# Kernel tuning notes

Hardware: AMD Instinct MI355X
Metric: run time of the kernel (lower is better)

The kernel has to match this reference:

```python
import jax, jax.numpy as jnp
import numpy as np

N_NODES = 100000
N_EDGES = 1600000
D_IN = 100      # entity/relation embedding dim (rel_weight is [100,50])
D_HID = 50      # conv1 out_channels (hard-coded in ctor)
N_REL = 237     # relation_num; rel_embedding doubled -> 474 relation types
N_REL2 = 2 * N_REL
N_BASES = 5     # num_bases hard-coded
N_CLASS = 50    # class_num


def setup_inputs() -> dict:
    key = jax.random.key(0)
    ks = jax.random.split(key, 12)
    x = jax.random.normal(ks[0], (N_NODES, D_IN), dtype=jnp.float32)
    edge_index = jax.random.randint(ks[1], (2, N_EDGES), 0, N_NODES)
    edge_type = jax.random.randint(ks[2], (N_EDGES,), 0, N_REL2)
    rel_embedding = jax.random.normal(ks[3], (N_REL, D_IN), dtype=jnp.float32) * 0.1
    rel_weight = jax.random.uniform(ks[4], (D_IN, D_HID), dtype=jnp.float32)  # nn.Parameter(torch.rand)
    basis1 = jax.random.normal(ks[5], (N_BASES, D_IN, D_HID), dtype=jnp.float32) * 0.1
    comp1 = jax.random.normal(ks[6], (N_REL2, N_BASES), dtype=jnp.float32) * 0.1
    root1 = jax.random.normal(ks[7], (D_IN, D_HID), dtype=jnp.float32) * 0.1
    bias1 = jnp.zeros((D_HID,), dtype=jnp.float32)
    basis2 = jax.random.normal(ks[8], (N_BASES, D_HID, N_CLASS), dtype=jnp.float32) * 0.1
    comp2 = jax.random.normal(ks[9], (N_REL2, N_BASES), dtype=jnp.float32) * 0.1
    root2 = jax.random.normal(ks[10], (D_HID, N_CLASS), dtype=jnp.float32) * 0.1
    bias2 = jnp.zeros((N_CLASS,), dtype=jnp.float32)
    return {
        "x": x, "edge_index": edge_index, "edge_type": edge_type, "target_node": 5,
        "rel_embedding": rel_embedding, "rel_weight": rel_weight,
        "basis1": basis1, "comp1": comp1, "root1": root1, "bias1": bias1,
        "basis2": basis2, "comp2": comp2, "root2": root2, "bias2": bias2,
    }


def _transe_conv(x, src, dst, e_emb, comp_e, basis, root_w, bias):
    """RGCN-style conv with TransE compose and basis decomposition.
    x: [N, Fin], e_emb: [E, Fin], comp_e: [E, B], basis: [B, Fin, Fout].
    message m = x[src] + e_emb; out_e = m @ (sum_b comp_e[b] * basis[b]); mean-agg at dst.
    """
    m = x[src] + e_emb  # [E, Fin] -- dominant gather
    acc = jnp.zeros((m.shape[0], basis.shape[2]), dtype=m.dtype)
    for b in range(basis.shape[0]):  # small fixed basis count (5)
        acc = acc + comp_e[:, b:b + 1] * (m @ basis[b])
    agg = jax.ops.segment_sum(acc, dst, num_segments=x.shape[0])  # [N, Fout]
    cnt = jax.ops.segment_sum(jnp.ones((dst.shape[0],), dtype=x.dtype), dst,
                              num_segments=x.shape[0])
    mean = agg / jnp.maximum(cnt, 1.0)[:, None]
    return mean + x @ root_w + bias


def reference(x, edge_index, edge_type, target_node, rel_embedding, rel_weight,
              basis1, comp1, root1, bias1, basis2, comp2, root2, bias2):
    # x[target_node] = 0
    x = x.at[target_node].set(0.0)
    src, dst = edge_index[0], edge_index[1]
    # rel_embedding doubled (forward + inverse relations)
    rel_full = jnp.concatenate([rel_embedding, rel_embedding], axis=0)  # [2R, D_IN]
    e1 = rel_full[edge_type]                                            # [E, D_IN]
    h = _transe_conv(x, src, dst, e1, comp1[edge_type], basis1, root1, bias1)
    rel2 = rel_full @ rel_weight                                        # [2R, D_HID]
    e2 = rel2[edge_type]                                                # [E, D_HID]
    h = _transe_conv(h, src, dst, e2, comp2[edge_type], basis2, root2, bias2)
    return jax.nn.log_softmax(h, axis=1)
```

## Files before the change

kernel.cpp:

```cpp
#include <hip/hip_runtime.h>
#include <hip/hip_bf16.h>

typedef __hip_bfloat16 bf16;

#define N_NODES 100000
#define N_EDGES 1600000
#define D_IN    100
#define D_HID   50
#define N_REL   237
#define N_REL2  474
#define N_CLASS 50

#define NBUCK    196
#define BSHIFT   9
#define BCAP     10240
#define BIN_EPB  1024
#define BIN_BLKS ((N_EDGES + BIN_EPB - 1) / BIN_EPB)

#define MID_PACK1_BLKS 160
#define MID_PACK2_BLKS 80
#define MID_REL_BLKS   474
#define MID_TOTAL (BIN_BLKS + MID_PACK1_BLKS + MID_PACK2_BLKS + MID_REL_BLKS)

#define GEMM_BLKS ((N_NODES + 31) / 32)

#define CST 324

#define RED_BLKS (N_NODES / 8)

typedef __attribute__((ext_vector_type(8))) short short8;
typedef __attribute__((ext_vector_type(4))) float f32x4;
typedef __attribute__((ext_vector_type(2))) float f32x2;

__device__ __forceinline__ float b2f(bf16 v) { return __bfloat162float(v); }
__device__ __forceinline__ bf16  f2b(float v) { return __float2bfloat16(v); }

__device__ __forceinline__ float ldw(const void* p, int idx, int isbf) {
    return isbf ? b2f(((const bf16*)p)[idx]) : ((const float*)p)[idx];
}

#if __has_builtin(__builtin_amdgcn_cvt_f32_fp8) && __has_builtin(__builtin_amdgcn_cvt_pk_fp8_f32)
#define F8_HW 1
#endif
#if __has_builtin(__builtin_amdgcn_cvt_pk_f32_fp8)
#define F8PK_HW 1
#endif

__device__ __forceinline__ float f8tof(unsigned u) {
#ifdef F8_HW
    return __builtin_amdgcn_cvt_f32_fp8((int)u, 0);
#else
    unsigned s = u >> 7, e = (u >> 3) & 0xF, m = u & 7;
    float v;
    if (e == 0) v = (float)m * 0.001953125f;
    else        v = (float)(8 + m) * __builtin_ldexpf(1.f, (int)e - 10);
    return s ? -v : v;
#endif
}

#ifdef F8_HW
#define F8SEL(u, s) __builtin_amdgcn_cvt_f32_fp8((int)(u), (s))
#else
#define F8SEL(u, s) f8tof(((u) >> (8 * (s))) & 0xFFu)
#endif

template <bool HI>
__device__ __forceinline__ f32x2 f8pk(unsigned u) {
#ifdef F8PK_HW
    return __builtin_amdgcn_cvt_pk_f32_fp8((int)u, HI);
#else
    f32x2 r;
    r.x = F8SEL(u, HI ? 2 : 0);
    r.y = F8SEL(u, HI ? 3 : 1);
    return r;
#endif
}

__device__ __forceinline__ unsigned f8enc_sw(float v) {
    unsigned bits = __float_as_uint(v);
    unsigned s = bits >> 31;
    float a = fabsf(v);
    if (a < 0.0009765625f) return s << 7;
    if (a >= 448.f) return (s << 7) | 0x7E;
    int E = (int)((bits >> 23) & 0xFF) - 127;
    unsigned m = bits & 0x7FFFFF;
    if (E < -6) {
        int q = (int)rintf(a * 512.f);
        if (q > 7) q = 7;
        return (s << 7) | (unsigned)q;
    }
    unsigned lsb = (m >> 20) & 1, rnd = (m >> 19) & 1;
    unsigned sticky = (m & 0x7FFFF) ? 1u : 0u;
    unsigned m3 = (m >> 20) + (rnd & (sticky | lsb));
    if (m3 == 8) { m3 = 0; E += 1; }
    if (E > 8) return (s << 7) | 0x7E;
    return (s << 7) | ((unsigned)(E + 7) << 3) | m3;
}

__device__ __forceinline__ unsigned pk4_f8(float v0, float v1, float v2, float v3) {
#ifdef F8_HW
    int p = __builtin_amdgcn_cvt_pk_fp8_f32(v0, v1, 0, false);
    p = __builtin_amdgcn_cvt_pk_fp8_f32(v2, v3, p, true);
    return (unsigned)p;
#else
    return f8enc_sw(v0) | (f8enc_sw(v1) << 8) | (f8enc_sw(v2) << 16) | (f8enc_sw(v3) << 24);
#endif
}

__global__ void k_detect(const unsigned short* __restrict__ xr, int* __restrict__ flag) {
    int tid = threadIdx.x;
    int cnt = 0;
    for (int i = tid; i < 4096; i += 256) {
        unsigned short u = xr[2 * i];
        unsigned e = (u >> 7) & 0xFF;
        bool pl = (e >= 107 && e <= 132) || ((u & 0x7FFF) == 0);
        cnt += pl ? 1 : 0;
    }
    __shared__ int sh[256];
    sh[tid] = cnt;
    __syncthreads();
    for (int s = 128; s > 0; s >>= 1) {
        if (tid < s) sh[tid] += sh[tid + s];
        __syncthreads();
    }
    if (tid == 0) flag[0] = (sh[0] >= 3072) ? 1 : 0;
}

__device__ __forceinline__ void job_bin(int blk, const int* __restrict__ src,
                                        const int* __restrict__ dst,
                                        const int* __restrict__ et,
                                        unsigned* __restrict__ bucketFill,
                                        unsigned long long* __restrict__ staging) {
    __shared__ unsigned lhist[NBUCK];
    __shared__ unsigned lstart[NBUCK];
    __shared__ unsigned gbase[NBUCK];
    __shared__ unsigned scan_tmp[NBUCK];
    __shared__ unsigned long long lval[BIN_EPB];
    __shared__ unsigned ltgt[BIN_EPB];
    int tid = threadIdx.x;
    int base = blk * BIN_EPB;
    int n = N_EDGES - base; if (n > BIN_EPB) n = BIN_EPB;

    for (int i = tid; i < NBUCK; i += 256) lhist[i] = 0;
    __syncthreads();

    unsigned bb[4], rr[4];
    unsigned long long vv[4];
#pragma unroll
    for (int j = 0; j < 4; ++j) {
        int i = j * 256 + tid;
        bb[j] = 0xFFFFFFFFu;
        if (i < n) {
            int e = base + i;
            unsigned d = (unsigned)dst[e];
            unsigned b = d >> BSHIFT;
            bb[j] = b;
            rr[j] = atomicAdd(&lhist[b], 1u);
            vv[j] = ((unsigned long long)d << 32) |
                    (unsigned long long)((unsigned)src[e] | ((unsigned)et[e] << 17));
        }
    }
    __syncthreads();
    unsigned v0 = (tid < NBUCK) ? lhist[tid] : 0;
    if (tid < NBUCK) scan_tmp[tid] = v0;
    __syncthreads();
    for (int s = 1; s < NBUCK; s <<= 1) {
        unsigned t = 0;
        if (tid < NBUCK && tid >= (unsigned)s) t = scan_tmp[tid - s];
        __syncthreads();
        if (tid < NBUCK) scan_tmp[tid] += t;
        __syncthreads();
    }
    if (tid < NBUCK) {
        lstart[tid] = scan_tmp[tid] - v0;
        gbase[tid] = (v0 > 0) ? atomicAdd(&bucketFill[tid], v0) : 0u;
    }
    __syncthreads();
#pragma unroll
    for (int j = 0; j < 4; ++j) {
        if (bb[j] != 0xFFFFFFFFu) {
            unsigned pos = lstart[bb[j]] + rr[j];
            unsigned off = gbase[bb[j]] + rr[j];
            lval[pos] = vv[j];
            ltgt[pos] = (off < BCAP) ? (bb[j] * BCAP + off) : 0xFFFFFFFFu;
        }
    }
    __syncthreads();
    for (int i = tid; i < n; i += 256) {
        unsigned t = ltgt[i];
        if (t != 0xFFFFFFFFu) staging[t] = lval[i];
    }
}

__device__ __forceinline__ void job_pack(int blk, const void* basis, const void* root,
                                         bf16* Wb, int KL, int isbf) {
    int g = blk * 256 + threadIdx.x;
    int ks = g / 10240;
    int r = g - ks * 10240;
    int ct = r >> 9;
    int r2 = r & 511;
    int l = r2 >> 3, j = r2 & 7;
    int k = ks * 32 + ((l >> 4) << 3) + j;
    int n = ct * 16 + (l & 15);
    float v = 0.f;
    if (k < KL && n < 300) {
        if (n < 250) { int b = n / 50, f = n - b * 50; v = ldw(basis, (b * KL + k) * 50 + f, isbf); }
        else         v = ldw(root, k * 50 + (n - 250), isbf);
    }
    Wb[g] = f2b(v);
}

template<int ISBF>
__device__ __forceinline__ void job_rel(int t,
        const void* __restrict__ rel_emb, const void* __restrict__ rel_w,
        const void* __restrict__ basis1, const void* __restrict__ comp1,
        const void* __restrict__ basis2, const void* __restrict__ comp2,
        float* __restrict__ rt1, float* __restrict__ rt2,
        float* __restrict__ c81, float* __restrict__ c82) {
    int tid = threadIdx.x;
    __shared__ float rf[D_IN];
    __shared__ float r2s[D_HID];
    int tm = (t >= N_REL) ? t - N_REL : t;
    if (tid < D_IN) rf[tid] = ldw(rel_emb, tm * D_IN + tid, ISBF);
    if (tid < 8) {
        c81[t * 8 + tid] = (tid < 5) ? ldw(comp1, t * 5 + tid, ISBF) : 0.f;
        c82[t * 8 + tid] = (tid < 5) ? ldw(comp2, t * 5 + tid, ISBF) : 0.f;
    }
    __syncthreads();
    if (tid < 50) {
        int f = tid;
        float a = 0.f;
        for (int b = 0; b < 5; ++b) {
            float cb = ldw(comp1, t * 5 + b, ISBF);
            float s = 0.f;
            for (int k = 0; k < D_IN; ++k) s += rf[k] * ldw(basis1, (b * D_IN + k) * 50 + f, ISBF);
            a += cb * s;
        }
        rt1[t * 50 + f] = a;
        float s2 = 0.f;
        for (int k = 0; k < D_IN; ++k) s2 += rf[k] * ldw(rel_w, k * 50 + f, ISBF);
        r2s[f] = s2;
    }
    __syncthreads();
    if (tid < 50) {
        int f = tid;
        float a = 0.f;
        for (int b = 0; b < 5; ++b) {
            float cb = ldw(comp2, t * 5 + b, ISBF);
            float s = 0.f;
            for (int k = 0; k < 50; ++k) s += r2s[k] * ldw(basis2, (b * 50 + k) * 50 + f, ISBF);
            a += cb * s;
        }
        rt2[t * 50 + f] = a;
    }
}

__global__ __launch_bounds__(256) void k_mid(const int* __restrict__ srcp,
                                             const int* __restrict__ dstp,
                                             const int* __restrict__ etp,
                                             unsigned* __restrict__ bucketFill,
                                             unsigned long long* __restrict__ staging,
                                             const int* __restrict__ flag,
                                             const void* rel_emb, const void* rel_w,
                                             const void* basis1, const void* comp1,
                                             const void* root1,
                                             const void* basis2, const void* comp2,
                                             const void* root2,
                                             bf16* __restrict__ Wb1, bf16* __restrict__ Wb2,
                                             float* __restrict__ rt1, float* __restrict__ rt2,
                                             float* __restrict__ c81, float* __restrict__ c82) {
    int blk = blockIdx.x;
    if (blk < BIN_BLKS) { job_bin(blk, srcp, dstp, etp, bucketFill, staging); return; }
    blk -= BIN_BLKS;
    int isbf = flag[0];
    if (blk < MID_PACK1_BLKS) { job_pack(blk, basis1, root1, Wb1, D_IN, isbf); return; }
    blk -= MID_PACK1_BLKS;
    if (blk < MID_PACK2_BLKS) { job_pack(blk, basis2, root2, Wb2, D_HID, isbf); return; }
    blk -= MID_PACK2_BLKS;
    if (isbf) job_rel<1>(blk, rel_emb, rel_w, basis1, comp1, basis2, comp2, rt1, rt2, c81, c82);
    else      job_rel<0>(blk, rel_emb, rel_w, basis1, comp1, basis2, comp2, rt1, rt2, c81, c82);
}

__device__ __forceinline__ void job_bucket(int b, char* shraw,
        const unsigned long long* __restrict__ staging,
        const unsigned* __restrict__ bucketFill,
        int* __restrict__ offs, unsigned* __restrict__ se) {
    unsigned* hist = (unsigned*)shraw;
    unsigned* excl = hist + 512;
    unsigned* bfs  = excl + 512;
    unsigned* tmp  = bfs + 256;
    int tid = threadIdx.x;

    if (tid < NBUCK) {
        unsigned c = bucketFill[tid];
        bfs[tid] = (c > BCAP) ? BCAP : c;
    }
    hist[tid] = 0; hist[tid + 256] = 0;
    __syncthreads();
    for (int s = 1; s < NBUCK; s <<= 1) {
        unsigned t = 0;
        if (tid < NBUCK && tid >= s) t = bfs[tid - s];
        __syncthreads();
        if (tid < NBUCK) bfs[tid] += t;
        __syncthreads();
    }
    unsigned base = (b == 0) ? 0u : bfs[b - 1];
    unsigned cnt = bfs[b] - base;

    const unsigned long long* p = staging + (size_t)b * BCAP;
    for (unsigned i = tid; i < cnt; i += 256) {
        unsigned d = (unsigned)(p[i] >> 32);
        atomicAdd(&hist[d & 511], 1u);
    }
    __syncthreads();
    unsigned h0 = hist[2 * tid], h1 = hist[2 * tid + 1];
    tmp[tid] = h0 + h1;
    __syncthreads();
    for (int s = 1; s < 256; s <<= 1) {
        unsigned t = (tid >= s) ? tmp[tid - s] : 0u;
        __syncthreads();
        tmp[tid] += t;
        __syncthreads();
    }
    unsigned pe = (tid > 0) ? tmp[tid - 1] : 0u;
    excl[2 * tid]     = pe;
    excl[2 * tid + 1] = pe + h0;
    hist[2 * tid] = 0; hist[2 * tid + 1] = 0;
    __syncthreads();

#pragma unroll
    for (int q = 0; q < 2; ++q) {
        int li = 2 * tid + q;
        int node = b * 512 + li;
        if (node < N_NODES) offs[node] = (int)(base + excl[li]);
        if (node == N_NODES - 1) offs[N_NODES] = (int)(base + cnt);
    }

    for (unsigned i = tid; i < cnt; i += 256) {
        unsigned long long v = p[i];
        unsigned ld = ((unsigned)(v >> 32)) & 511u;
        unsigned r = atomicAdd(&hist[ld], 1u);
        se[base + excl[ld] + r] = (unsigned)v;
    }
}

template<int KP, bool ZT, bool RAWX>
__global__ __launch_bounds__(256, 4) void k_gemm_b(const void* __restrict__ Xraw,
                                                const int* __restrict__ flag,
                                                const bf16* __restrict__ Wb,
                                                unsigned char* __restrict__ Y8,
                                                bf16* __restrict__ R, int M,
                                                const int* __restrict__ tgt,
                                                const unsigned long long* __restrict__ staging,
                                                const unsigned* __restrict__ bucketFill,
                                                int* __restrict__ offs,
                                                unsigned* __restrict__ se,
                                                int nbuckBlks) {
    constexpr int AP = KP + 8;
    constexpr int CBYTES = 32 * CST * 2;
    constexpr int ABYTES = 32 * AP * 2;
    __shared__ __attribute__((aligned(16))) char shraw[CBYTES + ABYTES];
    if ((int)blockIdx.x < nbuckBlks) {
        job_bucket(blockIdx.x, shraw, staging, bucketFill, offs, se);
        return;
    }
    int gblk = blockIdx.x - nbuckBlks;
    bf16* smemC = (bf16*)shraw;
    bf16* smemA = (bf16*)(shraw + CBYTES);
    int tid = threadIdx.x;
    int w = tid >> 6, lane = tid & 63;
    int quad = lane >> 4, cIn = lane & 15;
    int rw = w & 1, cw = w >> 1;
    int base_row = gblk * 32;

    if (RAWX) {
        int isbf = flag[0];
        for (int i = tid; i < 32 * 64; i += 256) {
            int r = i >> 6, c2 = (i & 63) << 1;
            int row = base_row + r; if (row > M - 1) row = M - 1;
            unsigned pkd = 0;
            if (c2 < 100) {
                if (isbf) {
                    pkd = *(const unsigned*)((const unsigned short*)Xraw + (size_t)row * 100 + c2);
                } else {
                    const float* xp = (const float*)Xraw + (size_t)row * 100 + c2;
                    float vx = xp[0], vy = xp[1];
                    bf16 b0 = f2b(vx), b1 = f2b(vy);
                    pkd = (unsigned)*(unsigned short*)&b0 | ((unsigned)*(unsigned short*)&b1 << 16);
                }
            }
            *(unsigned*)(&smemA[r * AP + c2]) = pkd;
        }
    } else {
        const bf16* X = (const bf16*)Xraw;
        const int TOT = 32 * KP / 8;
        for (int i = tid; i < TOT; i += 256) {
            int e8 = i * 8;
            int r = e8 / KP, c = e8 - r * KP;
            int row = base_row + r; if (row > M - 1) row = M - 1;
            *(uint4*)(&smemA[r * AP + c]) = *(const uint4*)(&X[(size_t)row * KP + c]);
        }
    }
    __syncthreads();

    f32x4 acc[10];
#pragma unroll
    for (int i = 0; i < 10; ++i) acc[i] = (f32x4){0.f, 0.f, 0.f, 0.f};

#pragma unroll
    for (int ks = 0; ks < KP / 32; ++ks) {
        short8 a = *(const short8*)(&smemA[(rw * 16 + cIn) * AP + ks * 32 + quad * 8]);
#pragma unroll
        for (int ct = 0; ct < 10; ++ct) {
            short8 b = *(const short8*)(&Wb[(size_t)((ks * 20 + cw * 10 + ct) * 64 + lane) * 8]);
            acc[ct] = __builtin_amdgcn_mfma_f32_16x16x32_bf16(a, b, acc[ct], 0, 0, 0);
        }
    }

#pragma unroll
    for (int ct = 0; ct < 10; ++ct)
#pragma unroll
        for (int r = 0; r < 4; ++r)
            smemC[(rw * 16 + quad * 4 + r) * CST + (cw * 10 + ct) * 16 + cIn] = f2b(acc[ct][r]);
    __syncthreads();

    int tv = -1;
    if (ZT) tv = tgt[0];
    int valid = M - base_row; if (valid > 32) valid = 32;

    for (int i = tid; i < valid * 64; i += 256) {
        int r = i >> 6, u = i & 63;
        int row = base_row + r;
        unsigned pbits;
        if (u < 50) {
            pbits = pk4_f8(b2f(smemC[r * CST + u]),       b2f(smemC[r * CST + 50 + u]),
                           b2f(smemC[r * CST + 100 + u]), b2f(smemC[r * CST + 150 + u]));
        } else if (u < 63) {
            int fb = (u - 50) * 4;
            float v0 = (fb + 0 < 50) ? b2f(smemC[r * CST + 200 + fb + 0]) : 0.f;
            float v1 = (fb + 1 < 50) ? b2f(smemC[r * CST + 200 + fb + 1]) : 0.f;
            float v2 = (fb + 2 < 50) ? b2f(smemC[r * CST + 200 + fb + 2]) : 0.f;
            float v3 = (fb + 3 < 50) ? b2f(smemC[r * CST + 200 + fb + 3]) : 0.f;
            pbits = pk4_f8(v0, v1, v2, v3);
        } else {
            pbits = 0u;
        }
        if (ZT && row == tv) pbits = 0u;
        *(unsigned*)(Y8 + (size_t)row * 256 + u * 4) = pbits;
    }
    for (int i = tid; i < valid * 32; i += 256) {
        int r = i >> 5, cu = i & 31;
        int row = base_row + r;
        int j0 = cu * 2, j1 = j0 + 1;
        unsigned short ua = (j0 < 50) ? *(const unsigned short*)&smemC[r * CST + 250 + j0] : 0;
        unsigned short ub = (j1 < 50) ? *(const unsigned short*)&smemC[r * CST + 250 + j1] : 0;
        unsigned u = (unsigned)ua | ((unsigned)ub << 16);
        if (ZT && row == tv) u = 0u;
        *(unsigned*)((unsigned short*)R + (size_t)row * 64 + j0) = u;
    }
}

__device__ __forceinline__ void edge_body(unsigned p, int f,
        const unsigned char* __restrict__ Y8,
        const float* __restrict__ c8, const float* __restrict__ rt,
        f32x2& acc2, float& accS) {
    unsigned ps = (unsigned)__builtin_amdgcn_readfirstlane((int)p);
    int s_ = (int)(ps & 0x1FFFFu);
    int t_ = (int)(ps >> 17);
    const unsigned char* yr = Y8 + (size_t)s_ * 256;
    unsigned a4 = *(const unsigned*)(yr + 4 * f);
    float y4 = f8tof(yr[200 + f]);
    const float* cp = c8 + t_ * 8;
    f32x4 c03 = *(const f32x4*)cp;
    float c4 = cp[4];
    float rv = rt[t_ * 50 + f];
    f32x2 y01 = f8pk<false>(a4);
    f32x2 y23 = f8pk<true>(a4);
    f32x2 cA; cA.x = c03.x; cA.y = c03.y;
    f32x2 cB; cB.x = c03.z; cB.y = c03.w;
    acc2 += cA * y01;
    acc2 += cB * y23;
    accS += rv + c4 * y4;
}

__device__ __forceinline__ void pair_reduce(const int* __restrict__ off,
        const unsigned int* __restrict__ se, const float* __restrict__ c8,
        const float* __restrict__ rt, const unsigned char* __restrict__ Y8,
        int rowA, int f, float& outA, float& outB, float& cntA, float& cntB) {
    int e0 = __builtin_amdgcn_readfirstlane(off[rowA]);
    int e1 = __builtin_amdgcn_readfirstlane(off[rowA + 1]);
    int e2 = __builtin_amdgcn_readfirstlane(off[rowA + 2]);
    f32x2 a2A; a2A.x = 0.f; a2A.y = 0.f;
    f32x2 a2B; a2B.x = 0.f; a2B.y = 0.f;
    float sA = 0.f, sB = 0.f;
    int eA = e0, eB = e1;
    while (eA + 4 <= e1 && eB + 4 <= e2) {
        unsigned pA0 = se[eA],     pA1 = se[eA + 1], pA2 = se[eA + 2], pA3 = se[eA + 3];
        unsigned pB0 = se[eB],     pB1 = se[eB + 1], pB2 = se[eB + 2], pB3 = se[eB + 3];
        edge_body(pA0, f, Y8, c8, rt, a2A, sA);
        edge_body(pB0, f, Y8, c8, rt, a2B, sB);
        edge_body(pA1, f, Y8, c8, rt, a2A, sA);
        edge_body(pB1, f, Y8, c8, rt, a2B, sB);
        edge_body(pA2, f, Y8, c8, rt, a2A, sA);
        edge_body(pB2, f, Y8, c8, rt, a2B, sB);
        edge_body(pA3, f, Y8, c8, rt, a2A, sA);
        edge_body(pB3, f, Y8, c8, rt, a2B, sB);
        eA += 4; eB += 4;
    }
    while (eA + 4 <= e1) {
        unsigned p0 = se[eA], p1 = se[eA + 1], p2 = se[eA + 2], p3 = se[eA + 3];
        edge_body(p0, f, Y8, c8, rt, a2A, sA);
        edge_body(p1, f, Y8, c8, rt, a2A, sA);
        edge_body(p2, f, Y8, c8, rt, a2A, sA);
        edge_body(p3, f, Y8, c8, rt, a2A, sA);
        eA += 4;
    }
    while (eB + 4 <= e2) {
        unsigned p0 = se[eB], p1 = se[eB + 1], p2 = se[eB + 2], p3 = se[eB + 3];
        edge_body(p0, f, Y8, c8, rt, a2B, sB);
        edge_body(p1, f, Y8, c8, rt, a2B, sB);
        edge_body(p2, f, Y8, c8, rt, a2B, sB);
        edge_body(p3, f, Y8, c8, rt, a2B, sB);
        eB += 4;
    }
    for (; eA < e1; ++eA) edge_body(se[eA], f, Y8, c8, rt, a2A, sA);
    for (; eB < e2; ++eB) edge_body(se[eB], f, Y8, c8, rt, a2B, sB);
    outA = a2A.x + a2A.y + sA;
    outB = a2B.x + a2B.y + sB;
    float nA = (float)(e1 - e0); cntA = nA > 1.f ? nA : 1.f;
    float nB = (float)(e2 - e1); cntB = nB > 1.f ? nB : 1.f;
}

__global__ __launch_bounds__(256) void k_reduce1(const int* __restrict__ off,
                                                 const unsigned int* __restrict__ se,
                                                 const float* __restrict__ c8,
                                                 const float* __restrict__ rt,
                                                 const unsigned char* __restrict__ Y8,
                                                 const bf16* __restrict__ R,
                                                 const void* __restrict__ bias_raw,
                                                 const int* __restrict__ flag,
                                                 bf16* __restrict__ h) {
    int wid = threadIdx.x >> 6, lane = threadIdx.x & 63;
    int rowA = __builtin_amdgcn_readfirstlane(blockIdx.x * 8 + wid * 2);
    int f = (lane < 50) ? lane : 49;
    float accA, accB, cntA, cntB;
    pair_reduce(off, se, c8, rt, Y8, rowA, f, accA, accB, cntA, cntB);
    float bv = ldw(bias_raw, f, flag[0]);
    float vA = accA / cntA + b2f(R[(size_t)rowA * 64 + f]) + bv;
    float vB = accB / cntB + b2f(R[(size_t)(rowA + 1) * 64 + f]) + bv;
    h[(size_t)rowA * 64 + lane]       = f2b(lane < 50 ? vA : 0.f);
    h[(size_t)(rowA + 1) * 64 + lane] = f2b(lane < 50 ? vB : 0.f);
}

__device__ __forceinline__ void softmax_store(float acc, float cnt, int row, int f,
        int lane, const bf16* __restrict__ R, float bv,
        int isbf, void* __restrict__ out) {
    float v = -INFINITY;
    if (lane < 50)
        v = acc / cnt + b2f(R[(size_t)row * 64 + f]) + bv;
    float m = v;
    for (int o = 32; o > 0; o >>= 1) m = fmaxf(m, __shfl_xor(m, o));
    float ex = (lane < 50) ? expf(v - m) : 0.f;
    float s = ex;
    for (int o = 32; o > 0; o >>= 1) s += __shfl_xor(s, o);
    float res = v - m - logf(s);
    if (lane < 50) {
        if (isbf) ((bf16*)out)[row * 50 + f] = f2b(res);
        else      ((float*)out)[row * 50 + f] = res;
    }
}

__global__ __launch_bounds__(256) void k_reduce2(const int* __restrict__ off,
                                                 const unsigned int* __restrict__ se,
                                                 const float* __restrict__ c8,
                                                 const float* __restrict__ rt,
                                                 const unsigned char* __restrict__ Y8,
                                                 const bf16* __restrict__ R,
                                                 const void* __restrict__ bias_raw,
                                                 const int* __restrict__ flag,
                                                 void* __restrict__ out) {
    int wid = threadIdx.x >> 6, lane = threadIdx.x & 63;
    int rowA = __builtin_amdgcn_readfirstlane(blockIdx.x * 8 + wid * 2);
    int f = (lane < 50) ? lane : 49;
    float accA, accB, cntA, cntB;
    pair_reduce(off, se, c8, rt, Y8, rowA, f, accA, accB, cntA, cntB);
    int isbf = flag[0];
    float bv = ldw(bias_raw, f, isbf);
    softmax_store(accA, cntA, rowA, f, lane, R, bv, isbf, out);
    softmax_store(accB, cntB, rowA + 1, f, lane, R, bv, isbf, out);
}

extern "C" void kernel_launch(void* const* d_in, const int* in_sizes, int n_in,
                              void* d_out, int out_size, void* d_ws, size_t ws_size,
                              hipStream_t stream) {
    const void* x_raw = d_in[0];
    const int*  ei    = (const int*)d_in[1];
    const int*  et    = (const int*)d_in[2];
    const int*  tgt   = (const int*)d_in[3];
    const void* rel_emb = d_in[4];
    const void* rel_w   = d_in[5];
    const void* basis1  = d_in[6];
    const void* comp1   = d_in[7];
    const void* root1   = d_in[8];
    const void* bias1   = d_in[9];
    const void* basis2  = d_in[10];
    const void* comp2   = d_in[11];
    const void* root2   = d_in[12];
    const void* bias2   = d_in[13];

    char* wsp = (char*)d_ws;
    size_t off_b = 0;
    auto alloc = [&](size_t bytes) {
        void* p = wsp + off_b;
        off_b = (off_b + bytes + 255) & ~(size_t)255;
        return p;
    };
    unsigned char* Y8 = (unsigned char*)alloc((size_t)N_NODES * 256);
    bf16*  R    = (bf16*) alloc((size_t)N_NODES * 64 * sizeof(bf16));
    bf16*  h    = (bf16*) alloc((size_t)N_NODES * 64 * sizeof(bf16));
    unsigned int* se = (unsigned int*)alloc((size_t)N_EDGES * sizeof(unsigned int));
    unsigned long long* staging = (unsigned long long*)alloc((size_t)NBUCK * BCAP * 8);
    int*   offs = (int*)  alloc((size_t)(N_NODES + 1) * sizeof(int));
    unsigned* bucketFill = (unsigned*)alloc((size_t)NBUCK * sizeof(unsigned));
    bf16*  Wb1  = (bf16*) alloc((size_t)40960 * sizeof(bf16));
    bf16*  Wb2  = (bf16*) alloc((size_t)20480 * sizeof(bf16));
    float* rt1  = (float*)alloc((size_t)N_REL2 * 50 * sizeof(float));
    float* rt2  = (float*)alloc((size_t)N_REL2 * 50 * sizeof(float));
    float* c81  = (float*)alloc((size_t)N_REL2 * 8 * sizeof(float));
    float* c82  = (float*)alloc((size_t)N_REL2 * 8 * sizeof(float));
    int*   flag = (int*)  alloc(sizeof(int));

    const int* srcp = ei;
    const int* dstp = ei + N_EDGES;

    hipMemsetAsync(bucketFill, 0, (size_t)NBUCK * sizeof(unsigned), stream);

    k_detect<<<1, 256, 0, stream>>>((const unsigned short*)x_raw, flag);

    k_mid<<<MID_TOTAL, 256, 0, stream>>>(srcp, dstp, et, bucketFill, staging, flag,
                                         rel_emb, rel_w, basis1, comp1, root1,
                                         basis2, comp2, root2,
                                         Wb1, Wb2, rt1, rt2, c81, c82);

    k_gemm_b<128, true, true><<<GEMM_BLKS + NBUCK, 256, 0, stream>>>(
        x_raw, flag, Wb1, Y8, R, N_NODES, tgt, staging, bucketFill, offs, se, NBUCK);

    k_reduce1<<<RED_BLKS, 256, 0, stream>>>(offs, se, c81, rt1, Y8, R, bias1, flag, h);

    k_gemm_b<64, false, false><<<GEMM_BLKS, 256, 0, stream>>>(
        h, flag, Wb2, Y8, R, N_NODES, nullptr, staging, bucketFill, offs, se, 0);

    k_reduce2<<<RED_BLKS, 256, 0, stream>>>(offs, se, c82, rt2, Y8, R, bias2, flag, d_out);
}
```

Before: 360.9 us.

## Fuse layer-1 mean aggregation with layer-2 basis GEMM into one kernel

Adds a 1024-thread kernel that runs the layer-1 edge reduction for 32 rows, keeps the resulting hidden activations in shared memory, and immediately multiplies them by the layer-2 basis weights with MFMA. It writes the fp8 Y and bf16 root outputs into separate ping-pong buffers, so no reads of layer-1 buffers are overwritten. This removes the global write and read of h and one kernel launch. The cost is extra workspace, used only when it fits, and large blocks that may limit occupancy during the latency-bound gather phase.

```diff
diff --git a/kernel.cpp b/kernel.cpp
--- a/kernel.cpp
+++ b/kernel.cpp
@@ -552,6 +552,89 @@
     h[(size_t)(rowA + 1) * 64 + lane] = f2b(lane < 50 ? vB : 0.f);
 }
 
+__global__ __launch_bounds__(1024) void k_fused(const int* __restrict__ off,
+                                                const unsigned int* __restrict__ se,
+                                                const float* __restrict__ c8,
+                                                const float* __restrict__ rt,
+                                                const unsigned char* __restrict__ Y8in,
+                                                const bf16* __restrict__ Rin,
+                                                const void* __restrict__ bias_raw,
+                                                const int* __restrict__ flag,
+                                                const bf16* __restrict__ Wb,
+                                                unsigned char* __restrict__ Y8out,
+                                                bf16* __restrict__ Rout) {
+    constexpr int HP = 72;
+    __shared__ __attribute__((aligned(16))) char shraw[32 * HP * 2 + 32 * CST * 2];
+    bf16* hT    = (bf16*)shraw;
+    bf16* smemC = (bf16*)(shraw + 32 * HP * 2);
+    int tid = threadIdx.x;
+    int wid = tid >> 6, lane = tid & 63;
+    int quad = lane >> 4, cIn = lane & 15;
+    int base_row = blockIdx.x * 32;
+    int rowA = __builtin_amdgcn_readfirstlane(base_row + wid * 2);
+    int f = (lane < 50) ? lane : 49;
+
+    float accA, accB, cntA, cntB;
+    pair_reduce(off, se, c8, rt, Y8in, rowA, f, accA, accB, cntA, cntB);
+    float bv = ldw(bias_raw, f, flag[0]);
+    float vA = accA / cntA + b2f(Rin[(size_t)rowA * 64 + f]) + bv;
+    float vB = accB / cntB + b2f(Rin[(size_t)(rowA + 1) * 64 + f]) + bv;
+    hT[(wid * 2) * HP + lane]     = f2b(lane < 50 ? vA : 0.f);
+    hT[(wid * 2 + 1) * HP + lane] = f2b(lane < 50 ? vB : 0.f);
+    __syncthreads();
+
+    if (wid < 8) {
+        int rw = wid & 1, cs = wid >> 1;
+        f32x4 acc[5];
+#pragma unroll
+        for (int i = 0; i < 5; ++i) acc[i] = (f32x4){0.f, 0.f, 0.f, 0.f};
+#pragma unroll
+        for (int ks = 0; ks < 2; ++ks) {
+            short8 a = *(const short8*)(&hT[(rw * 16 + cIn) * HP + ks * 32 + quad * 8]);
+#pragma unroll
+            for (int j = 0; j < 5; ++j) {
+                short8 b = *(const short8*)(&Wb[(size_t)((ks * 20 + cs * 5 + j) * 64 + lane) * 8]);
+                acc[j] = __builtin_amdgcn_mfma_f32_16x16x32_bf16(a, b, acc[j], 0, 0, 0);
+            }
+        }
+#pragma unroll
+        for (int j = 0; j < 5; ++j)
+#pragma unroll
+            for (int r = 0; r < 4; ++r)
+                smemC[(rw * 16 + quad * 4 + r) * CST + (cs * 5 + j) * 16 + cIn] = f2b(acc[j][r]);
+    }
+    __syncthreads();
+
+    for (int i = tid; i < 32 * 64; i += 1024) {
+        int r = i >> 6, u = i & 63;
+        int row = base_row + r;
+        unsigned pbits;
+        if (u < 50) {
+            pbits = pk4_f8(b2f(smemC[r * CST + u]),       b2f(smemC[r * CST + 50 + u]),
+                           b2f(smemC[r * CST + 100 + u]), b2f(smemC[r * CST + 150 + u]));
+        } else if (u < 63) {
+            int fb = (u - 50) * 4;
+            float v0 = (fb + 0 < 50) ? b2f(smemC[r * CST + 200 + fb + 0]) : 0.f;
+            float v1 = (fb + 1 < 50) ? b2f(smemC[r * CST + 200 + fb + 1]) : 0.f;
+            float v2 = (fb + 2 < 50) ? b2f(smemC[r * CST + 200 + fb + 2]) : 0.f;
+            float v3 = (fb + 3 < 50) ? b2f(smemC[r * CST + 200 + fb + 3]) : 0.f;
+            pbits = pk4_f8(v0, v1, v2, v3);
+        } else {
+            pbits = 0u;
+        }
+        *(unsigned*)(Y8out + (size_t)row * 256 + u * 4) = pbits;
+    }
+    for (int i = tid; i < 32 * 32; i += 1024) {
+        int r = i >> 5, cu = i & 31;
+        int row = base_row + r;
+        int j0 = cu * 2, j1 = j0 + 1;
+        unsigned short ua = (j0 < 50) ? *(const unsigned short*)&smemC[r * CST + 250 + j0] : 0;
+        unsigned short ub = (j1 < 50) ? *(const unsigned short*)&smemC[r * CST + 250 + j1] : 0;
+        unsigned u = (unsigned)ua | ((unsigned)ub << 16);
+        *(unsigned*)((unsigned short*)Rout + (size_t)row * 64 + j0) = u;
+    }
+}
+
 __device__ __forceinline__ void softmax_store(float acc, float cnt, int row, int f,
         int lane, const bf16* __restrict__ R, float bv,
         int isbf, void* __restrict__ out) {
@@ -617,7 +700,6 @@
     };
     unsigned char* Y8 = (unsigned char*)alloc((size_t)N_NODES * 256);
     bf16*  R    = (bf16*) alloc((size_t)N_NODES * 64 * sizeof(bf16));
-    bf16*  h    = (bf16*) alloc((size_t)N_NODES * 64 * sizeof(bf16));
     unsigned int* se = (unsigned int*)alloc((size_t)N_EDGES * sizeof(unsigned int));
     unsigned long long* staging = (unsigned long long*)alloc((size_t)NBUCK * BCAP * 8);
     int*   offs = (int*)  alloc((size_t)(N_NODES + 1) * sizeof(int));
@@ -630,6 +712,16 @@
     float* c82  = (float*)alloc((size_t)N_REL2 * 8 * sizeof(float));
     int*   flag = (int*)  alloc(sizeof(int));
 
+    size_t fusedExtra = (size_t)N_NODES * 256 + 512 + (size_t)N_NODES * 64 * 2 + 512;
+    bool useFused = (off_b + fusedExtra <= ws_size);
+    unsigned char* Y8b = nullptr; bf16* Rb = nullptr; bf16* h = nullptr;
+    if (useFused) {
+        Y8b = (unsigned char*)alloc((size_t)N_NODES * 256);
+        Rb  = (bf16*)alloc((size_t)N_NODES * 64 * sizeof(bf16));
+    } else {
+        h   = (bf16*)alloc((size_t)N_NODES * 64 * sizeof(bf16));
+    }
+
     const int* srcp = ei;
     const int* dstp = ei + N_EDGES;
 
@@ -645,10 +737,14 @@
     k_gemm_b<128, true, true><<<GEMM_BLKS + NBUCK, 256, 0, stream>>>(
         x_raw, flag, Wb1, Y8, R, N_NODES, tgt, staging, bucketFill, offs, se, NBUCK);
 
-    k_reduce1<<<RED_BLKS, 256, 0, stream>>>(offs, se, c81, rt1, Y8, R, bias1, flag, h);
-
-    k_gemm_b<64, false, false><<<GEMM_BLKS, 256, 0, stream>>>(
-        h, flag, Wb2, Y8, R, N_NODES, nullptr, staging, bucketFill, offs, se, 0);
-
-    k_reduce2<<<RED_BLKS, 256, 0, stream>>>(offs, se, c82, rt2, Y8, R, bias2, flag, d_out);
-}
+    if (useFused) {
+        k_fused<<<GEMM_BLKS, 1024, 0, stream>>>(offs, se, c81, rt1, Y8, R, bias1, flag,
+                                                Wb2, Y8b, Rb);
+        k_reduce2<<<RED_BLKS, 256, 0, stream>>>(offs, se, c82, rt2, Y8b, Rb, bias2, flag, d_out);
+    } else {
+        k_reduce1<<<RED_BLKS, 256, 0, stream>>>(offs, se, c81, rt1, Y8, R, bias1, flag, h);
+        k_gemm_b<64, false, false><<<GEMM_BLKS, 256, 0, stream>>>(
+            h, flag, Wb2, Y8, R, N_NODES, nullptr, staging, bucketFill, offs, se, 0);
+        k_reduce2<<<RED_BLKS, 256, 0, stream>>>(offs, se, c82, rt2, Y8, R, bias2, flag, d_out);
+    }
+}
```

After: 392.4 us. +8.7%, slower.
